# Optimization experiments

Hardware: AMD Instinct MI355X
Metric: run time of the kernel (lower is better)

The kernel has to match this reference:

```python
import jax, jax.numpy as jnp
import numpy as np
from functools import partial

OUT = 11  # out_channels of both MDLSTM layers
NDIR = 4  # Graves MDLSTM: 4 scan directions (2 per axis); height==1 so vertical neighbor is always the zero boundary state


def mdlstm(x, W, U, b):
    """Multi-directional LSTM over a height-1 strip.
    x: (B, Cin, 1, Wd); W: (4, Cin, 5*OUT); U: (4, OUT, 5*OUT); b: (4, 5*OUT)
    Gates per step: [i, f_w, f_h, o, a]. With height==1 the vertical cell state
    is the zero boundary, so the f_h branch contributes nothing.
    Returns (B, 4, OUT, 1, Wd).
    """
    B, Cin, _, Wd = x.shape
    xs = jnp.transpose(x[:, :, 0, :], (0, 2, 1))          # (B, Wd, Cin)
    xr = xs[:, ::-1, :]                                    # width-reversed
    xd = jnp.stack([xs, xr, xs, xr], axis=0)               # (4, B, Wd, Cin)
    # Precompute input contribution to all gates for every step.
    gx = jnp.einsum('dbwc,dcg->wdbg', xd, W) + b[None, :, None, :]  # (Wd,4,B,5*OUT)

    def step(carry, g_t):
        h, c = carry                                       # each (4, B, OUT)
        g = g_t + jnp.einsum('dbo,dog->dbg', h, U)         # (4, B, 5*OUT)
        i, f_w, f_h, o, a = jnp.split(g, 5, axis=-1)
        i = jax.nn.sigmoid(i)
        f_w = jax.nn.sigmoid(f_w)
        o = jax.nn.sigmoid(o)
        a = jnp.tanh(a)
        c_new = i * a + f_w * c                            # + sigmoid(f_h) * 0 (vertical boundary)
        h_new = o * jnp.tanh(c_new)
        return (h_new, c_new), h_new

    init = (jnp.zeros((NDIR, B, OUT), x.dtype), jnp.zeros((NDIR, B, OUT), x.dtype))
    _, hs = jax.lax.scan(step, init, gx)                   # (Wd, 4, B, OUT)
    h = jnp.transpose(hs, (2, 1, 3, 0))                    # (B, 4, OUT, Wd)
    # un-reverse the right-to-left directions
    h = h.at[:, 1].set(h[:, 1, :, ::-1]).at[:, 3].set(h[:, 3, :, ::-1])
    return h[:, :, :, None, :]                             # (B, 4, OUT, 1, Wd)


def setup_inputs() -> dict:
    key = jax.random.key(0)
    ks = jax.random.split(key, 7)
    B, H, Wd = 256, 32, 2048
    s = 0.1
    return {
        'x':  jax.random.normal(ks[0], (B, 1, H, Wd), jnp.float32),
        'W0': s * jax.random.normal(ks[1], (NDIR, 1,   5 * OUT), jnp.float32),
        'U0': s * jax.random.normal(ks[2], (NDIR, OUT, 5 * OUT), jnp.float32),
        'b0': jnp.zeros((NDIR, 5 * OUT), jnp.float32),
        'W1': s * jax.random.normal(ks[3], (NDIR, OUT, 5 * OUT), jnp.float32),
        'U1': s * jax.random.normal(ks[4], (NDIR, OUT, 5 * OUT), jnp.float32),
        'b1': jnp.zeros((NDIR, 5 * OUT), jnp.float32),
    }


def reference(x, W0, U0, b0, W1, U1, b1):
    x = x.sum(axis=2, keepdims=True)                       # (B, 1, 1, Wd)
    y = mdlstm(x, W0, U0, b0).sum(axis=1)                  # (B, 11, 1, Wd): sum over directions
    y = mdlstm(y, W1, U1, b1).sum(axis=1)                  # (B, 11, 1, Wd)
    return y[:, :, 0, :]                                   # (B, 11, Wd)
```

## Files before the change

### kernel.cpp

```cpp
#include <hip/hip_runtime.h>
#include <hip/hip_bf16.h>


#define NOUT 11
#define WD 2048
#define NB 256
#define ROW 12
#define ACCN (WD * ROW)
#define YROW 6
#define YPAD 12
#define YBFN (WD * YROW + 2 * YPAD)

#define NTHR 1024
#define NCK 4
#define CHUNK 512
#define WARM 64

typedef float f2 __attribute__((ext_vector_type(2)));
typedef float f4 __attribute__((ext_vector_type(4)));
typedef unsigned int u32;
typedef u32 u32x2 __attribute__((ext_vector_type(2)));
typedef __fp16 h2 __attribute__((ext_vector_type(2)));

#define LOG2E 1.4426950408889634f

union UH { u32 u; h2 h; };
__device__ __forceinline__ u32 h2u(h2 v) { UH x; x.h = v; return x.u; }
__device__ __forceinline__ h2 u2h(u32 v) { UH x; x.u = v; return x.h; }

__device__ __forceinline__ h2 rlh(h2 v, int l) {
  return u2h((u32)__builtin_amdgcn_readlane((int)h2u(v), l));
}
template <int CTRL>
__device__ __forceinline__ float dppf(float v) {
  return __int_as_float(__builtin_amdgcn_update_dpp(
      __float_as_int(v), __float_as_int(v), CTRL, 0xF, 0xF, false));
}
__device__ __forceinline__ float rcp_(float x) { return __builtin_amdgcn_rcpf(x); }
__device__ __forceinline__ float exp2_(float x) { return __builtin_amdgcn_exp2f(x); }
__device__ __forceinline__ float dot2(h2 a, h2 b, float c) {
  return __builtin_amdgcn_fdot2(a, b, c, false);
}

#define STEP(DOACC, ...)                                                       \
  do {                                                                         \
    const float hnx = dppf<0x104>(hj);      \
    const h2 hpk = __builtin_amdgcn_cvt_pkrtz(hj, hnx);                        \
    const h2 hp0 = rlh(hpk, 0);                                                \
    const h2 hp1 = rlh(hpk, 8);                                                \
    const h2 hp2 = rlh(hpk, 16);                                               \
    const h2 hp3 = rlh(hpk, 24);                                               \
    const h2 hp4 = rlh(hpk, 32);                                               \
    const h2 hp5 = rlh(hpk, 40);                                               \
    __VA_ARGS__                                                                \
    float g = dot2(hp0, Up[0], gi);                                            \
    g = dot2(hp1, Up[1], g);                                                   \
    g = dot2(hp2, Up[2], g);                                                   \
    g = dot2(hp3, Up[3], g);                                                   \
    g = dot2(hp4, Up[4], g);                                                   \
    g = dot2(hp5, Up[5], g);                                                   \
    const float sg = rcp_(1.0f + exp2_(g));                                    \
    const float act = fmaf(kA, sg, kB);                                        \
    const float fv = dppf<0x55>(act);                                          \
    const float ov = dppf<0xAA>(act);                                          \
    const float av = dppf<0xFF>(act);                                          \
    const float ov2 = ov + ov;                                  \
    cpr = fmaf(fv, cpr, act * av);           \
    const float r2t = rcp_(1.0f + exp2_(cpr));                                 \
    hj = fmaf(ov2, r2t, -ov);            \
    if (DOACC && wr0) atomicAdd(&acc[ao], hj);                                 \
    ao += ad;                                                                  \
  } while (0)

__global__ __launch_bounds__(NTHR, 1) void mdlstm_fused(
    const float* __restrict__ x, const float* __restrict__ W0,
    const float* __restrict__ U0, const float* __restrict__ b0,
    const float* __restrict__ W1, const float* __restrict__ U1,
    const float* __restrict__ b1, float* __restrict__ out) {
  __shared__ __align__(16) float acc[ACCN];
  __shared__ __align__(16) u32 ybf[YBFN];

  const int tid = threadIdx.x;
  const int b = blockIdx.x;
  float* xw = (float*)ybf;

  {
    const f4* xb4 = (const f4*)(x + (size_t)b * 32 * WD);
    f4* xw4 = (f4*)xw;
    for (int w = tid; w < WD / 4; w += NTHR) {
      f4 s = xb4[w];
#pragma unroll
      for (int h = 1; h < 32; ++h) s += xb4[h * (WD / 4) + w];
      xw4[w] = s;
    }
    f4* a4 = (f4*)acc;
    const f4 z = {0.f, 0.f, 0.f, 0.f};
    for (int i = tid; i < ACCN / 4; i += NTHR) a4[i] = z;
  }
  __syncthreads();

  const int lane = tid & 63;
  const int wv = tid >> 6;
  const int d = wv & 3;
  const int ck = wv >> 2;
  const bool fwd = ((d & 1) == 0);
  const int warm = (ck == 0) ? 0 : WARM;
  const int base = ck * CHUNK;
  const int j = lane >> 2;
  const int cls = lane & 3;
  const bool wr0 = (cls == 0);
  const int colb = (cls == 0) ? 0 : (cls == 1) ? 11 : (cls == 2) ? 33 : 44;
  const int colc = (j < NOUT) ? (colb + j) : 54;
  const float scl =
      ((cls == 3) ? -2.0f * LOG2E : -LOG2E) * ((j < NOUT) ? 1.0f : 0.0f);
  const float kA = (cls == 3) ? (-4.0f * LOG2E) : 1.0f;
  const float kB = (cls == 3) ? (2.0f * LOG2E) : 0.0f;

  if (lane < 48) {
    float uv[12];
#pragma unroll
    for (int s = 0; s < NOUT; ++s) uv[s] = U0[(d * NOUT + s) * 55 + colc] * scl;
    uv[11] = 0.f;
    h2 Up[6];
#pragma unroll
    for (int k = 0; k < 6; ++k)
      Up[k] = __builtin_amdgcn_cvt_pkrtz(uv[2 * k], uv[2 * k + 1]);
    const float Wcs = W0[d * 55 + colc] * scl;
    const float bcs = b0[d * 55 + colc] * scl;

    const int p0 = fwd ? (base - warm) : (WD - 1 - base + warm);
    int xo = p0;
    const int xd = fwd ? 1 : -1;
    int ao = p0 * ROW + j;
    const int ad = fwd ? ROW : -ROW;

    float hj = 0.f;
    float cpr = 0.f;
    float gi_next = 0.f;
    const float xc = xw[xo & (WD - 1)];
    xo += xd;
    float gi = fmaf(xc, Wcs, bcs);
    float xn = xw[xo & (WD - 1)];
    xo += xd;

#define PREP1                                                                  \
    const float xn2 = xw[xo & (WD - 1)];         \
    xo += xd;                                                                  \
    gi_next = fmaf(xn, Wcs, bcs);                         \
    xn = xn2;

    for (int t = 0; t < warm; t += 2) {
      STEP(0, PREP1);
      gi = gi_next;
      STEP(0, PREP1);
      gi = gi_next;
    }
    for (int t = 0; t < CHUNK; t += 2) {
      STEP(1, PREP1);
      gi = gi_next;
      STEP(1, PREP1);
      gi = gi_next;
    }
#undef PREP1
  }
  __syncthreads();

  {
    const f2* a2 = (const f2*)acc;
    for (int i = tid; i < WD * YROW; i += NTHR) {
      const f2 v = a2[i];
      ybf[YPAD + i] = h2u(__builtin_amdgcn_cvt_pkrtz(v.x, v.y));
    }
    if (tid < YPAD) {
      ybf[tid] = 0;
      ybf[WD * YROW + YPAD + tid] = 0;
    }
  }
  __syncthreads();
  {
    f4* a4 = (f4*)acc;
    const f4 z = {0.f, 0.f, 0.f, 0.f};
    for (int i = tid; i < ACCN / 4; i += NTHR) a4[i] = z;
  }
  __syncthreads();

  if (lane < 48) {
    float uv[12], wvv[12];
#pragma unroll
    for (int s = 0; s < NOUT; ++s) {
      uv[s] = U1[(d * NOUT + s) * 55 + colc] * scl;
      wvv[s] = W1[(d * NOUT + s) * 55 + colc] * scl;
    }
    uv[11] = 0.f;
    wvv[11] = 0.f;
    h2 Up[6], Wp[6];
#pragma unroll
    for (int k = 0; k < 6; ++k) {
      Up[k] = __builtin_amdgcn_cvt_pkrtz(uv[2 * k], uv[2 * k + 1]);
      Wp[k] = __builtin_amdgcn_cvt_pkrtz(wvv[2 * k], wvv[2 * k + 1]);
    }
    const float bcs = b1[d * 55 + colc] * scl;

    const u32x2* yv = (const u32x2*)ybf;
    const int p0 = fwd ? (base - warm) : (WD - 1 - base + warm);
    const int qd = fwd ? 3 : -3;
    int q = 3 * p0 + 6;

    auto GI = [&](u32x2 r0, u32x2 r1, u32x2 r2) -> float {
      float A = dot2(u2h(r0.x), Wp[0], bcs);
      A = dot2(u2h(r0.y), Wp[1], A);
      A = dot2(u2h(r1.x), Wp[2], A);
      A = dot2(u2h(r1.y), Wp[3], A);
      A = dot2(u2h(r2.x), Wp[4], A);
      A = dot2(u2h(r2.y), Wp[5], A);
      return A;
    };

    u32x2 c0 = yv[q];
    u32x2 c1 = yv[q + 1];
    u32x2 c2 = yv[q + 2];
    q += qd;
    u32x2 pr0 = yv[q];
    u32x2 pr1 = yv[q + 1];
    u32x2 pr2 = yv[q + 2];
    q += qd;

    float gi = GI(c0, c1, c2);

    int ao = p0 * ROW + j;
    const int ad = fwd ? ROW : -ROW;

    float hj = 0.f;
    float cpr = 0.f;
    float gi_next = 0.f;

#define PREP2                                                                  \
    const u32x2 n0 = yv[q];                  \
    const u32x2 n1 = yv[q + 1];                                                \
    const u32x2 n2 = yv[q + 2];                                                \
    q += qd;                                                                   \
    gi_next = GI(pr0, pr1, pr2);                          \
    pr0 = n0;                                                                  \
    pr1 = n1;                                                                  \
    pr2 = n2;

    for (int t = 0; t < warm; t += 2) {
      STEP(0, PREP2);
      gi = gi_next;
      STEP(0, PREP2);
      gi = gi_next;
    }
    for (int t = 0; t < CHUNK; t += 2) {
      STEP(1, PREP2);
      gi = gi_next;
      STEP(1, PREP2);
      gi = gi_next;
    }
#undef PREP2
  }
  __syncthreads();

  float* ob = out + (size_t)b * (NOUT * WD);
  for (int i = tid; i < NOUT * WD; i += NTHR) {
    const int jj = i >> 11;
    const int w = i & (WD - 1);
    ob[i] = acc[w * ROW + jj];
  }
}

extern "C" void kernel_launch(void* const* d_in, const int* in_sizes, int n_in,
                              void* d_out, int out_size, void* d_ws,
                              size_t ws_size, hipStream_t stream) {
  const float* x  = (const float*)d_in[0];
  const float* W0 = (const float*)d_in[1];
  const float* U0 = (const float*)d_in[2];
  const float* b0 = (const float*)d_in[3];
  const float* W1 = (const float*)d_in[4];
  const float* U1 = (const float*)d_in[5];
  const float* b1 = (const float*)d_in[6];
  float* out = (float*)d_out;

  mdlstm_fused<<<NB, NTHR, 0, stream>>>(x, W0, U0, b0, W1, U1, b1, out);
}
```

Baseline: 464.5 us.

## Pack two chunks per wave with two gates per lane and bpermute broadcast

Each wave now splits into two 32-lane halves, each scanning a separate chunk, which doubles the chunk count and halves the chunk length. Each lane computes two gate columns instead of one, and the per-step h broadcast uses ds_bpermute instead of readlane, so both halves get their own hidden state. The intent is to shorten the serial recurrence per wave by half. The cost is more warm-up overhead, since every chunk including chunk zero runs a warm-up and then resets, plus more LDS permute latency on the critical path.

```diff
diff --git a/kernel.cpp b/kernel.cpp
--- a/kernel.cpp
+++ b/kernel.cpp
@@ -12,8 +12,8 @@
 #define YBFN (WD * YROW + 2 * YPAD)
 
 #define NTHR 1024
-#define NCK 4
-#define CHUNK 512
+#define NCK 8
+#define CHUNK 256
 #define WARM 64
 
 typedef float f2 __attribute__((ext_vector_type(2)));
@@ -28,9 +28,6 @@
 __device__ __forceinline__ u32 h2u(h2 v) { UH x; x.h = v; return x.u; }
 __device__ __forceinline__ h2 u2h(u32 v) { UH x; x.u = v; return x.h; }
 
-__device__ __forceinline__ h2 rlh(h2 v, int l) {
-  return u2h((u32)__builtin_amdgcn_readlane((int)h2u(v), l));
-}
 template <int CTRL>
 __device__ __forceinline__ float dppf(float v) {
   return __int_as_float(__builtin_amdgcn_update_dpp(
@@ -41,34 +38,43 @@
 __device__ __forceinline__ float dot2(h2 a, h2 b, float c) {
   return __builtin_amdgcn_fdot2(a, b, c, false);
 }
+__device__ __forceinline__ h2 bperm(int addr, h2 src) {
+  return u2h((u32)__builtin_amdgcn_ds_bpermute(addr, (int)h2u(src)));
+}
 
 #define STEP(DOACC, ...)                                                       \
   do {                                                                         \
-    const float hnx = dppf<0x104>(hj);      \
-    const h2 hpk = __builtin_amdgcn_cvt_pkrtz(hj, hnx);                        \
-    const h2 hp0 = rlh(hpk, 0);                                                \
-    const h2 hp1 = rlh(hpk, 8);                                                \
-    const h2 hp2 = rlh(hpk, 16);                                               \
-    const h2 hp3 = rlh(hpk, 24);                                               \
-    const h2 hp4 = rlh(hpk, 32);                                               \
-    const h2 hp5 = rlh(hpk, 40);                                               \
+    const float hsh = dppf<0x102>(hj);      \
+    const h2 hpk = __builtin_amdgcn_cvt_pkrtz(hj, hsh);                        \
+    const h2 hp0 = bperm(bpa0, hpk);       \
+    const h2 hp1 = bperm(bpa1, hpk);                                           \
+    const h2 hp2 = bperm(bpa2, hpk);                                           \
+    const h2 hp3 = bperm(bpa3, hpk);                                           \
+    const h2 hp4 = bperm(bpa4, hpk);                                           \
+    const h2 hp5 = bperm(bpa5, hpk);                                           \
     __VA_ARGS__                                                                \
-    float g = dot2(hp0, Up[0], gi);                                            \
-    g = dot2(hp1, Up[1], g);                                                   \
-    g = dot2(hp2, Up[2], g);                                                   \
-    g = dot2(hp3, Up[3], g);                                                   \
-    g = dot2(hp4, Up[4], g);                                                   \
-    g = dot2(hp5, Up[5], g);                                                   \
-    const float sg = rcp_(1.0f + exp2_(g));                                    \
-    const float act = fmaf(kA, sg, kB);                                        \
-    const float fv = dppf<0x55>(act);                                          \
-    const float ov = dppf<0xAA>(act);                                          \
-    const float av = dppf<0xFF>(act);                                          \
-    const float ov2 = ov + ov;                                  \
-    cpr = fmaf(fv, cpr, act * av);           \
+    float gA = dot2(hp0, UpA[0], giA);                                         \
+    gA = dot2(hp1, UpA[1], gA);                                                \
+    gA = dot2(hp2, UpA[2], gA);                                                \
+    gA = dot2(hp3, UpA[3], gA);                                                \
+    gA = dot2(hp4, UpA[4], gA);                                                \
+    gA = dot2(hp5, UpA[5], gA);                                                \
+    float gB = dot2(hp0, UpB[0], giB);                                         \
+    gB = dot2(hp1, UpB[1], gB);                                                \
+    gB = dot2(hp2, UpB[2], gB);                                                \
+    gB = dot2(hp3, UpB[3], gB);                                                \
+    gB = dot2(hp4, UpB[4], gB);                                                \
+    gB = dot2(hp5, UpB[5], gB);                                                \
+    const float sA = rcp_(1.0f + exp2_(gA));      \
+    const float sB = rcp_(1.0f + exp2_(gB));                                   \
+    const float actB = fmaf(kABv, sB, kBBv);     \
+    const float swA = dppf<0xB1>(sA);        \
+    const float swB = dppf<0xB1>(actB);                          \
+    const float ov2 = actB + actB;                              \
+    cpr = fmaf(swA, cpr, sA * swB);           \
     const float r2t = rcp_(1.0f + exp2_(cpr));                                 \
-    hj = fmaf(ov2, r2t, -ov);            \
-    if (DOACC && wr0) atomicAdd(&acc[ao], hj);                                 \
+    hj = fmaf(ov2, r2t, -actB);                          \
+    if (DOACC && wr) atomicAdd(&acc[ao], hj);                                  \
     ao += ad;                                                                  \
   } while (0)
 
@@ -101,65 +107,84 @@
 
   const int lane = tid & 63;
   const int wv = tid >> 6;
+  const int half = lane >> 5;
   const int d = wv & 3;
-  const int ck = wv >> 2;
+  const int ck = (wv >> 2) + (half << 2);
   const bool fwd = ((d & 1) == 0);
-  const int warm = (ck == 0) ? 0 : WARM;
   const int base = ck * CHUNK;
-  const int j = lane >> 2;
-  const int cls = lane & 3;
-  const bool wr0 = (cls == 0);
-  const int colb = (cls == 0) ? 0 : (cls == 1) ? 11 : (cls == 2) ? 33 : 44;
-  const int colc = (j < NOUT) ? (colb + j) : 54;
-  const float scl =
-      ((cls == 3) ? -2.0f * LOG2E : -LOG2E) * ((j < NOUT) ? 1.0f : 0.0f);
-  const float kA = (cls == 3) ? (-4.0f * LOG2E) : 1.0f;
-  const float kB = (cls == 3) ? (2.0f * LOG2E) : 0.0f;
-
-  if (lane < 48) {
-    float uv[12];
-#pragma unroll
-    for (int s = 0; s < NOUT; ++s) uv[s] = U0[(d * NOUT + s) * 55 + colc] * scl;
-    uv[11] = 0.f;
-    h2 Up[6];
-#pragma unroll
-    for (int k = 0; k < 6; ++k)
-      Up[k] = __builtin_amdgcn_cvt_pkrtz(uv[2 * k], uv[2 * k + 1]);
-    const float Wcs = W0[d * 55 + colc] * scl;
-    const float bcs = b0[d * 55 + colc] * scl;
-
-    const int p0 = fwd ? (base - warm) : (WD - 1 - base + warm);
+  const int j = (lane & 31) >> 1;
+  const int gc = lane & 1;
+  const bool real = (j <= 10);
+  const bool wr = (gc == 0) && real;
+  const bool ck0z = (ck == 0);
+  const int colA = real ? ((gc == 0) ? j : 11 + j) : 54;
+  const int colB = real ? ((gc == 0) ? 33 + j : 44 + j) : 54;
+  const float sclA = real ? -LOG2E : 0.f;
+  const float sclB = real ? ((gc == 0) ? -LOG2E : -2.f * LOG2E) : 0.f;
+  const float kABv = (gc == 0) ? 1.f : (-4.f * LOG2E);
+  const float kBBv = (gc == 0) ? 0.f : (2.f * LOG2E);
+  const int bpa0 = ((lane & 32) << 2);
+  const int bpa1 = bpa0 + 16;
+  const int bpa2 = bpa0 + 32;
+  const int bpa3 = bpa0 + 48;
+  const int bpa4 = bpa0 + 64;
+  const int bpa5 = bpa0 + 80;
+
+  const int p0 = fwd ? (base - WARM) : (WD - 1 - base + WARM);
+  const int xd = fwd ? 1 : -1;
+  const int ad = fwd ? ROW : -ROW;
+  const int qd = fwd ? 3 : -3;
+
+  {
+    float uvA[12], uvB[12];
+#pragma unroll
+    for (int s = 0; s < NOUT; ++s) {
+      uvA[s] = U0[(d * NOUT + s) * 55 + colA] * sclA;
+      uvB[s] = U0[(d * NOUT + s) * 55 + colB] * sclB;
+    }
+    uvA[11] = 0.f;
+    uvB[11] = 0.f;
+    h2 UpA[6], UpB[6];
+#pragma unroll
+    for (int k = 0; k < 6; ++k) {
+      UpA[k] = __builtin_amdgcn_cvt_pkrtz(uvA[2 * k], uvA[2 * k + 1]);
+      UpB[k] = __builtin_amdgcn_cvt_pkrtz(uvB[2 * k], uvB[2 * k + 1]);
+    }
+    const float WcsA = W0[d * 55 + colA] * sclA;
+    const float bcsA = b0[d * 55 + colA] * sclA;
+    const float WcsB = W0[d * 55 + colB] * sclB;
+    const float bcsB = b0[d * 55 + colB] * sclB;
+
     int xo = p0;
-    const int xd = fwd ? 1 : -1;
     int ao = p0 * ROW + j;
-    const int ad = fwd ? ROW : -ROW;
-
-    float hj = 0.f;
-    float cpr = 0.f;
-    float gi_next = 0.f;
+    float hj = 0.f, cpr = 0.f, gnA = 0.f, gnB = 0.f;
     const float xc = xw[xo & (WD - 1)];
     xo += xd;
-    float gi = fmaf(xc, Wcs, bcs);
+    float giA = fmaf(xc, WcsA, bcsA);
+    float giB = fmaf(xc, WcsB, bcsB);
     float xn = xw[xo & (WD - 1)];
     xo += xd;
 
 #define PREP1                                                                  \
     const float xn2 = xw[xo & (WD - 1)];         \
     xo += xd;                                                                  \
-    gi_next = fmaf(xn, Wcs, bcs);                         \
+    gnA = fmaf(xn, WcsA, bcsA);                           \
+    gnB = fmaf(xn, WcsB, bcsB);                                                \
     xn = xn2;
 
-    for (int t = 0; t < warm; t += 2) {
+    for (int t = 0; t < WARM; t += 2) {
       STEP(0, PREP1);
-      gi = gi_next;
+      giA = gnA; giB = gnB;
       STEP(0, PREP1);
-      gi = gi_next;
-    }
+      giA = gnA; giB = gnB;
+    }
+    hj = ck0z ? 0.f : hj;
+    cpr = ck0z ? 0.f : cpr;
     for (int t = 0; t < CHUNK; t += 2) {
       STEP(1, PREP1);
-      gi = gi_next;
+      giA = gnA; giB = gnB;
       STEP(1, PREP1);
-      gi = gi_next;
+      giA = gnA; giB = gnB;
     }
 #undef PREP1
   }
@@ -184,35 +209,46 @@
   }
   __syncthreads();
 
-  if (lane < 48) {
-    float uv[12], wvv[12];
+  {
+    float uvA[12], uvB[12], wvA[12], wvB[12];
 #pragma unroll
     for (int s = 0; s < NOUT; ++s) {
-      uv[s] = U1[(d * NOUT + s) * 55 + colc] * scl;
-      wvv[s] = W1[(d * NOUT + s) * 55 + colc] * scl;
-    }
-    uv[11] = 0.f;
-    wvv[11] = 0.f;
-    h2 Up[6], Wp[6];
+      uvA[s] = U1[(d * NOUT + s) * 55 + colA] * sclA;
+      uvB[s] = U1[(d * NOUT + s) * 55 + colB] * sclB;
+      wvA[s] = W1[(d * NOUT + s) * 55 + colA] * sclA;
+      wvB[s] = W1[(d * NOUT + s) * 55 + colB] * sclB;
+    }
+    uvA[11] = uvB[11] = wvA[11] = wvB[11] = 0.f;
+    h2 UpA[6], UpB[6], WpA[6], WpB[6];
 #pragma unroll
     for (int k = 0; k < 6; ++k) {
-      Up[k] = __builtin_amdgcn_cvt_pkrtz(uv[2 * k], uv[2 * k + 1]);
-      Wp[k] = __builtin_amdgcn_cvt_pkrtz(wvv[2 * k], wvv[2 * k + 1]);
-    }
-    const float bcs = b1[d * 55 + colc] * scl;
+      UpA[k] = __builtin_amdgcn_cvt_pkrtz(uvA[2 * k], uvA[2 * k + 1]);
+      UpB[k] = __builtin_amdgcn_cvt_pkrtz(uvB[2 * k], uvB[2 * k + 1]);
+      WpA[k] = __builtin_amdgcn_cvt_pkrtz(wvA[2 * k], wvA[2 * k + 1]);
+      WpB[k] = __builtin_amdgcn_cvt_pkrtz(wvB[2 * k], wvB[2 * k + 1]);
+    }
+    const float bcsA = b1[d * 55 + colA] * sclA;
+    const float bcsB = b1[d * 55 + colB] * sclB;
 
     const u32x2* yv = (const u32x2*)ybf;
-    const int p0 = fwd ? (base - warm) : (WD - 1 - base + warm);
-    const int qd = fwd ? 3 : -3;
     int q = 3 * p0 + 6;
 
-    auto GI = [&](u32x2 r0, u32x2 r1, u32x2 r2) -> float {
-      float A = dot2(u2h(r0.x), Wp[0], bcs);
-      A = dot2(u2h(r0.y), Wp[1], A);
-      A = dot2(u2h(r1.x), Wp[2], A);
-      A = dot2(u2h(r1.y), Wp[3], A);
-      A = dot2(u2h(r2.x), Wp[4], A);
-      A = dot2(u2h(r2.y), Wp[5], A);
+    auto GIA = [&](u32x2 r0, u32x2 r1, u32x2 r2) -> float {
+      float A = dot2(u2h(r0.x), WpA[0], bcsA);
+      A = dot2(u2h(r0.y), WpA[1], A);
+      A = dot2(u2h(r1.x), WpA[2], A);
+      A = dot2(u2h(r1.y), WpA[3], A);
+      A = dot2(u2h(r2.x), WpA[4], A);
+      A = dot2(u2h(r2.y), WpA[5], A);
+      return A;
+    };
+    auto GIB = [&](u32x2 r0, u32x2 r1, u32x2 r2) -> float {
+      float A = dot2(u2h(r0.x), WpB[0], bcsB);
+      A = dot2(u2h(r0.y), WpB[1], A);
+      A = dot2(u2h(r1.x), WpB[2], A);
+      A = dot2(u2h(r1.y), WpB[3], A);
+      A = dot2(u2h(r2.x), WpB[4], A);
+      A = dot2(u2h(r2.y), WpB[5], A);
       return A;
     };
 
@@ -225,36 +261,36 @@
     u32x2 pr2 = yv[q + 2];
     q += qd;
 
-    float gi = GI(c0, c1, c2);
+    float giA = GIA(c0, c1, c2);
+    float giB = GIB(c0, c1, c2);
 
     int ao = p0 * ROW + j;
-    const int ad = fwd ? ROW : -ROW;
-
-    float hj = 0.f;
-    float cpr = 0.f;
-    float gi_next = 0.f;
+    float hj = 0.f, cpr = 0.f, gnA = 0.f, gnB = 0.f;
 
 #define PREP2                                                                  \
     const u32x2 n0 = yv[q];                  \
     const u32x2 n1 = yv[q + 1];                                                \
     const u32x2 n2 = yv[q + 2];                                                \
     q += qd;                                                                   \
-    gi_next = GI(pr0, pr1, pr2);                          \
+    gnA = GIA(pr0, pr1, pr2);                             \
+    gnB = GIB(pr0, pr1, pr2);                                                  \
     pr0 = n0;                                                                  \
     pr1 = n1;                                                                  \
     pr2 = n2;
 
-    for (int t = 0; t < warm; t += 2) {
+    for (int t = 0; t < WARM; t += 2) {
       STEP(0, PREP2);
-      gi = gi_next;
+      giA = gnA; giB = gnB;
       STEP(0, PREP2);
-      gi = gi_next;
-    }
+      giA = gnA; giB = gnB;
+    }
+    hj = ck0z ? 0.f : hj;
+    cpr = ck0z ? 0.f : cpr;
     for (int t = 0; t < CHUNK; t += 2) {
       STEP(1, PREP2);
-      gi = gi_next;
+      giA = gnA; giB = gnB;
       STEP(1, PREP2);
-      gi = gi_next;
+      giA = gnA; giB = gnB;
     }
 #undef PREP2
   }
```

After: 555.2 us. 1.2x slower.

## Map one chain per 16-lane group with all four gates per lane, halve chunk

Applied to the files above, without the earlier changes.

Restructures the recurrence so each 16-lane group owns one scan chain and each lane computes all four gates for one hidden unit, replacing cross-lane DPP gate exchange and readlane broadcasts with ds_swizzle within the group. It also halves the block to 512 threads while doubling the number of width chunks to 8 of 256 steps. Chunk 0 now runs warm-up steps too, with the state reset afterwards, so all chains stay uniform. This shortens the serial dependency chain per block, at the cost of quadrupled dot-product work per lane, more registers, and more warm-up overhead.

```diff
diff --git a/kernel.cpp b/kernel.cpp
--- a/kernel.cpp
+++ b/kernel.cpp
@@ -11,9 +11,9 @@
 #define YPAD 12
 #define YBFN (WD * YROW + 2 * YPAD)
 
-#define NTHR 1024
-#define NCK 4
-#define CHUNK 512
+#define NTHR 512
+#define NCK 8
+#define CHUNK 256
 #define WARM 64
 
 typedef float f2 __attribute__((ext_vector_type(2)));
@@ -28,14 +28,15 @@
 __device__ __forceinline__ u32 h2u(h2 v) { UH x; x.h = v; return x.u; }
 __device__ __forceinline__ h2 u2h(u32 v) { UH x; x.u = v; return x.h; }
 
-__device__ __forceinline__ h2 rlh(h2 v, int l) {
-  return u2h((u32)__builtin_amdgcn_readlane((int)h2u(v), l));
-}
 template <int CTRL>
 __device__ __forceinline__ float dppf(float v) {
   return __int_as_float(__builtin_amdgcn_update_dpp(
       __float_as_int(v), __float_as_int(v), CTRL, 0xF, 0xF, false));
 }
+template <int IMM>
+__device__ __forceinline__ h2 swzh(h2 v) {
+  return u2h((u32)__builtin_amdgcn_ds_swizzle((int)h2u(v), IMM));
+}
 __device__ __forceinline__ float rcp_(float x) { return __builtin_amdgcn_rcpf(x); }
 __device__ __forceinline__ float exp2_(float x) { return __builtin_amdgcn_exp2f(x); }
 __device__ __forceinline__ float dot2(h2 a, h2 b, float c) {
@@ -44,31 +45,49 @@
 
 #define STEP(DOACC, ...)                                                       \
   do {                                                                         \
-    const float hnx = dppf<0x104>(hj);      \
-    const h2 hpk = __builtin_amdgcn_cvt_pkrtz(hj, hnx);                        \
-    const h2 hp0 = rlh(hpk, 0);                                                \
-    const h2 hp1 = rlh(hpk, 8);                                                \
-    const h2 hp2 = rlh(hpk, 16);                                               \
-    const h2 hp3 = rlh(hpk, 24);                                               \
-    const h2 hp4 = rlh(hpk, 32);                                               \
-    const h2 hp5 = rlh(hpk, 40);                                               \
+    const float hnx = dppf<0x101>(hj);   \
+    const h2 hpk = __builtin_amdgcn_cvt_pkrtz(hj, hnx);   \
+    const h2 hp0 = swzh<0x010>(hpk);                      \
+    const h2 hp1 = swzh<0x050>(hpk);                                  \
+    const h2 hp2 = swzh<0x090>(hpk);                                  \
+    const h2 hp3 = swzh<0x0D0>(hpk);                                  \
+    const h2 hp4 = swzh<0x110>(hpk);                                  \
+    const h2 hp5 = swzh<0x150>(hpk);                                 \
     __VA_ARGS__                                                                \
-    float g = dot2(hp0, Up[0], gi);                                            \
-    g = dot2(hp1, Up[1], g);                                                   \
-    g = dot2(hp2, Up[2], g);                                                   \
-    g = dot2(hp3, Up[3], g);                                                   \
-    g = dot2(hp4, Up[4], g);                                                   \
-    g = dot2(hp5, Up[5], g);                                                   \
-    const float sg = rcp_(1.0f + exp2_(g));                                    \
-    const float act = fmaf(kA, sg, kB);                                        \
-    const float fv = dppf<0x55>(act);                                          \
-    const float ov = dppf<0xAA>(act);                                          \
-    const float av = dppf<0xFF>(act);                                          \
-    const float ov2 = ov + ov;                                  \
-    cpr = fmaf(fv, cpr, act * av);           \
-    const float r2t = rcp_(1.0f + exp2_(cpr));                                 \
-    hj = fmaf(ov2, r2t, -ov);            \
-    if (DOACC && wr0) atomicAdd(&acc[ao], hj);                                 \
+    float gI = dot2(hp0, UpI[0], giI);                                         \
+    gI = dot2(hp1, UpI[1], gI);                                                \
+    gI = dot2(hp2, UpI[2], gI);                                                \
+    gI = dot2(hp3, UpI[3], gI);                                                \
+    gI = dot2(hp4, UpI[4], gI);                                                \
+    gI = dot2(hp5, UpI[5], gI);                                                \
+    float gF = dot2(hp0, UpF[0], giF);                                         \
+    gF = dot2(hp1, UpF[1], gF);                                                \
+    gF = dot2(hp2, UpF[2], gF);                                                \
+    gF = dot2(hp3, UpF[3], gF);                                                \
+    gF = dot2(hp4, UpF[4], gF);                                                \
+    gF = dot2(hp5, UpF[5], gF);                                                \
+    float gO = dot2(hp0, UpO[0], giO);                                         \
+    gO = dot2(hp1, UpO[1], gO);                                                \
+    gO = dot2(hp2, UpO[2], gO);                                                \
+    gO = dot2(hp3, UpO[3], gO);                                                \
+    gO = dot2(hp4, UpO[4], gO);                                                \
+    gO = dot2(hp5, UpO[5], gO);                                                \
+    float gA = dot2(hp0, UpA[0], giA);                                         \
+    gA = dot2(hp1, UpA[1], gA);                                                \
+    gA = dot2(hp2, UpA[2], gA);                                                \
+    gA = dot2(hp3, UpA[3], gA);                                                \
+    gA = dot2(hp4, UpA[4], gA);                                                \
+    gA = dot2(hp5, UpA[5], gA);                                                \
+    const float sI = rcp_(1.0f + exp2_(gI));                                   \
+    const float sF = rcp_(1.0f + exp2_(gF));                                   \
+    const float sO = rcp_(1.0f + exp2_(gO));                                   \
+    const float sA = rcp_(1.0f + exp2_(gA));                                   \
+    const float taS = fmaf(-4.0f * LOG2E, sA, 2.0f * LOG2E);     \
+    cpr = fmaf(sF, cpr, sI * taS);                      \
+    const float r2t = rcp_(1.0f + exp2_(cpr));                  \
+    const float sO2 = sO + sO;                                                 \
+    hj = fmaf(sO2, r2t, -sO);                                 \
+    if (DOACC && wr) atomicAdd(&acc[ao], hj);                                  \
     ao += ad;                                                                  \
   } while (0)
 
@@ -101,65 +120,88 @@
 
   const int lane = tid & 63;
   const int wv = tid >> 6;
-  const int d = wv & 3;
-  const int ck = wv >> 2;
+  const int grp = lane >> 4;
+  const int u = lane & 15;
+  const int chain = wv * 4 + grp;
+  const int d = chain & 3;
+  const int ck = chain >> 2;
   const bool fwd = ((d & 1) == 0);
-  const int warm = (ck == 0) ? 0 : WARM;
   const int base = ck * CHUNK;
-  const int j = lane >> 2;
-  const int cls = lane & 3;
-  const bool wr0 = (cls == 0);
-  const int colb = (cls == 0) ? 0 : (cls == 1) ? 11 : (cls == 2) ? 33 : 44;
-  const int colc = (j < NOUT) ? (colb + j) : 54;
-  const float scl =
-      ((cls == 3) ? -2.0f * LOG2E : -LOG2E) * ((j < NOUT) ? 1.0f : 0.0f);
-  const float kA = (cls == 3) ? (-4.0f * LOG2E) : 1.0f;
-  const float kB = (cls == 3) ? (2.0f * LOG2E) : 0.0f;
-
-  if (lane < 48) {
+  const bool real = (u <= 10);
+  const bool wr = real;
+  const bool ck0z = (ck == 0);
+  const int colI = real ? u : 54;
+  const int colF = real ? (11 + u) : 54;
+  const int colO = real ? (33 + u) : 54;
+  const int colA = real ? (44 + u) : 54;
+  const float sclS = real ? -LOG2E : 0.f;
+  const float sclA = real ? (-2.f * LOG2E) : 0.f;
+
+  const int p0 = fwd ? (base - WARM) : (WD - 1 - base + WARM);
+  const int xd = fwd ? 1 : -1;
+  const int ad = fwd ? ROW : -ROW;
+  const int qd = fwd ? 3 : -3;
+
+  auto loadU = [&](const float* U, int col, float scl, h2* Up) {
     float uv[12];
 #pragma unroll
-    for (int s = 0; s < NOUT; ++s) uv[s] = U0[(d * NOUT + s) * 55 + colc] * scl;
+    for (int s = 0; s < NOUT; ++s) uv[s] = U[(d * NOUT + s) * 55 + col] * scl;
     uv[11] = 0.f;
-    h2 Up[6];
 #pragma unroll
     for (int k = 0; k < 6; ++k)
       Up[k] = __builtin_amdgcn_cvt_pkrtz(uv[2 * k], uv[2 * k + 1]);
-    const float Wcs = W0[d * 55 + colc] * scl;
-    const float bcs = b0[d * 55 + colc] * scl;
-
-    const int p0 = fwd ? (base - warm) : (WD - 1 - base + warm);
+  };
+
+  {
+    h2 UpI[6], UpF[6], UpO[6], UpA[6];
+    loadU(U0, colI, sclS, UpI);
+    loadU(U0, colF, sclS, UpF);
+    loadU(U0, colO, sclS, UpO);
+    loadU(U0, colA, sclA, UpA);
+    const float WcI = W0[d * 55 + colI] * sclS;
+    const float WcF = W0[d * 55 + colF] * sclS;
+    const float WcO = W0[d * 55 + colO] * sclS;
+    const float WcA = W0[d * 55 + colA] * sclA;
+    const float bcI = b0[d * 55 + colI] * sclS;
+    const float bcF = b0[d * 55 + colF] * sclS;
+    const float bcO = b0[d * 55 + colO] * sclS;
+    const float bcA = b0[d * 55 + colA] * sclA;
+
     int xo = p0;
-    const int xd = fwd ? 1 : -1;
-    int ao = p0 * ROW + j;
-    const int ad = fwd ? ROW : -ROW;
-
-    float hj = 0.f;
-    float cpr = 0.f;
-    float gi_next = 0.f;
+    int ao = p0 * ROW + u;
+    float hj = 0.f, cpr = 0.f;
+    float gnI = 0.f, gnF = 0.f, gnO = 0.f, gnA = 0.f;
     const float xc = xw[xo & (WD - 1)];
     xo += xd;
-    float gi = fmaf(xc, Wcs, bcs);
+    float giI = fmaf(xc, WcI, bcI);
+    float giF = fmaf(xc, WcF, bcF);
+    float giO = fmaf(xc, WcO, bcO);
+    float giA = fmaf(xc, WcA, bcA);
     float xn = xw[xo & (WD - 1)];
     xo += xd;
 
 #define PREP1                                                                  \
     const float xn2 = xw[xo & (WD - 1)];         \
     xo += xd;                                                                  \
-    gi_next = fmaf(xn, Wcs, bcs);                         \
+    gnI = fmaf(xn, WcI, bcI);                             \
+    gnF = fmaf(xn, WcF, bcF);                                                  \
+    gnO = fmaf(xn, WcO, bcO);                                                  \
+    gnA = fmaf(xn, WcA, bcA);                                                  \
     xn = xn2;
 
-    for (int t = 0; t < warm; t += 2) {
+    for (int t = 0; t < WARM; t += 2) {
       STEP(0, PREP1);
-      gi = gi_next;
+      giI = gnI; giF = gnF; giO = gnO; giA = gnA;
       STEP(0, PREP1);
-      gi = gi_next;
-    }
+      giI = gnI; giF = gnF; giO = gnO; giA = gnA;
+    }
+    hj = ck0z ? 0.f : hj;
+    cpr = ck0z ? 0.f : cpr;
     for (int t = 0; t < CHUNK; t += 2) {
       STEP(1, PREP1);
-      gi = gi_next;
+      giI = gnI; giF = gnF; giO = gnO; giA = gnA;
       STEP(1, PREP1);
-      gi = gi_next;
+      giI = gnI; giF = gnF; giO = gnO; giA = gnA;
     }
 #undef PREP1
   }
@@ -184,30 +226,28 @@
   }
   __syncthreads();
 
-  if (lane < 48) {
-    float uv[12], wvv[12];
-#pragma unroll
-    for (int s = 0; s < NOUT; ++s) {
-      uv[s] = U1[(d * NOUT + s) * 55 + colc] * scl;
-      wvv[s] = W1[(d * NOUT + s) * 55 + colc] * scl;
-    }
-    uv[11] = 0.f;
-    wvv[11] = 0.f;
-    h2 Up[6], Wp[6];
-#pragma unroll
-    for (int k = 0; k < 6; ++k) {
-      Up[k] = __builtin_amdgcn_cvt_pkrtz(uv[2 * k], uv[2 * k + 1]);
-      Wp[k] = __builtin_amdgcn_cvt_pkrtz(wvv[2 * k], wvv[2 * k + 1]);
-    }
-    const float bcs = b1[d * 55 + colc] * scl;
+  {
+    h2 UpI[6], UpF[6], UpO[6], UpA[6];
+    h2 WpI[6], WpF[6], WpO[6], WpA[6];
+    loadU(U1, colI, sclS, UpI);
+    loadU(U1, colF, sclS, UpF);
+    loadU(U1, colO, sclS, UpO);
+    loadU(U1, colA, sclA, UpA);
+    loadU(W1, colI, sclS, WpI);
+    loadU(W1, colF, sclS, WpF);
+    loadU(W1, colO, sclS, WpO);
+    loadU(W1, colA, sclA, WpA);
+    const float bcI = b1[d * 55 + colI] * sclS;
+    const float bcF = b1[d * 55 + colF] * sclS;
+    const float bcO = b1[d * 55 + colO] * sclS;
+    const float bcA = b1[d * 55 + colA] * sclA;
 
     const u32x2* yv = (const u32x2*)ybf;
-    const int p0 = fwd ? (base - warm) : (WD - 1 - base + warm);
-    const int qd = fwd ? 3 : -3;
     int q = 3 * p0 + 6;
 
-    auto GI = [&](u32x2 r0, u32x2 r1, u32x2 r2) -> float {
-      float A = dot2(u2h(r0.x), Wp[0], bcs);
+    auto GIc = [&](const h2* Wp, float bc, u32x2 r0, u32x2 r1,
+                   u32x2 r2) -> float {
+      float A = dot2(u2h(r0.x), Wp[0], bc);
       A = dot2(u2h(r0.y), Wp[1], A);
       A = dot2(u2h(r1.x), Wp[2], A);
       A = dot2(u2h(r1.y), Wp[3], A);
@@ -225,36 +265,41 @@
     u32x2 pr2 = yv[q + 2];
     q += qd;
 
-    float gi = GI(c0, c1, c2);
-
-    int ao = p0 * ROW + j;
-    const int ad = fwd ? ROW : -ROW;
-
-    float hj = 0.f;
-    float cpr = 0.f;
-    float gi_next = 0.f;
+    float giI = GIc(WpI, bcI, c0, c1, c2);
+    float giF = GIc(WpF, bcF, c0, c1, c2);
+    float giO = GIc(WpO, bcO, c0, c1, c2);
+    float giA = GIc(WpA, bcA, c0, c1, c2);
+
+    int ao = p0 * ROW + u;
+    float hj = 0.f, cpr = 0.f;
+    float gnI = 0.f, gnF = 0.f, gnO = 0.f, gnA = 0.f;
 
 #define PREP2                                                                  \
     const u32x2 n0 = yv[q];                  \
     const u32x2 n1 = yv[q + 1];                                                \
     const u32x2 n2 = yv[q + 2];                                                \
     q += qd;                                                                   \
-    gi_next = GI(pr0, pr1, pr2);                          \
+    gnI = GIc(WpI, bcI, pr0, pr1, pr2);                   \
+    gnF = GIc(WpF, bcF, pr0, pr1, pr2);                                        \
+    gnO = GIc(WpO, bcO, pr0, pr1, pr2);                                        \
+    gnA = GIc(WpA, bcA, pr0, pr1, pr2);                                        \
     pr0 = n0;                                                                  \
     pr1 = n1;                                                                  \
     pr2 = n2;
 
-    for (int t = 0; t < warm; t += 2) {
+    for (int t = 0; t < WARM; t += 2) {
       STEP(0, PREP2);
-      gi = gi_next;
+      giI = gnI; giF = gnF; giO = gnO; giA = gnA;
       STEP(0, PREP2);
-      gi = gi_next;
-    }
+      giI = gnI; giF = gnF; giO = gnO; giA = gnA;
+    }
+    hj = ck0z ? 0.f : hj;
+    cpr = ck0z ? 0.f : cpr;
     for (int t = 0; t < CHUNK; t += 2) {
       STEP(1, PREP2);
-      gi = gi_next;
+      giI = gnI; giF = gnF; giO = gnO; giA = gnA;
       STEP(1, PREP2);
-      gi = gi_next;
+      giI = gnI; giF = gnF; giO = gnO; giA = gnA;
     }
 #undef PREP2
   }
```

New measurement: 477.4 us. 1.03x slower.
